# Kernel optimization log

Measured on AMD Instinct MI355X. Metric: run time of the kernel, lower is better.

## Reference

```python
import jax, jax.numpy as jnp
import numpy as np

B, T, D_IN, D_OUT = 128, 2048, 128, 256


def setup_inputs() -> dict:
    key = jax.random.key(0)
    ks = jax.random.split(key, 8)
    s_in = 1.0 / np.sqrt(D_IN)
    s_h = 1.0 / np.sqrt(D_OUT)
    def orth(k):
        a = jax.random.normal(k, (D_OUT, D_OUT), dtype=jnp.float32)
        q, _ = jnp.linalg.qr(a)
        return q.astype(jnp.float32)
    return {
        "x": jax.random.normal(ks[0], (B, T, D_IN), dtype=jnp.float32),
        "h0": jnp.zeros((B, D_OUT), dtype=jnp.float32),
        "Wz": jax.random.normal(ks[1], (D_IN, D_OUT), dtype=jnp.float32) * s_in,
        "Wr": jax.random.normal(ks[2], (D_IN, D_OUT), dtype=jnp.float32) * s_in,
        "Wx": jax.random.normal(ks[3], (D_IN, D_OUT), dtype=jnp.float32) * s_in,
        "Uh": orth(ks[4]),
        "Rz": orth(ks[5]),
        "Rr": orth(ks[6]),
        "Bz": jnp.zeros((D_OUT,), dtype=jnp.float32),
        "Br": jnp.zeros((D_OUT,), dtype=jnp.float32),
        "Bh": jnp.zeros((D_OUT,), dtype=jnp.float32),
    }


def _mod_relu(zi, bi):
    # zi / |zi| * relu(|zi| + bi)  (faithful to the original modReLU)
    a = jnp.abs(zi)
    return zi / a * jax.nn.relu(a + bi)


def reference(x, h0, Wz, Wr, Wx, Uh, Rz, Rr, Bz, Br, Bh):
    # Precompute input projections for all timesteps in three big GEMMs.
    xz = jnp.einsum('btd,dh->bth', x, Wz) + Bz  # [B,T,H]
    xr = jnp.einsum('btd,dh->bth', x, Wr) + Br
    xx = jnp.einsum('btd,dh->bth', x, Wx)

    def step(h, xs):
        xz_t, xr_t, xx_t = xs
        zt = jax.nn.sigmoid(xz_t + h @ Rz)
        rt = jax.nn.sigmoid(xr_t + h @ Rr)
        zi = xx_t + rt * (h @ Uh)
        h_new = zt * h + (1.0 - zt) * _mod_relu(zi, Bh)
        return h_new, h_new

    # scan over time: move T to leading axis
    xs = (jnp.swapaxes(xz, 0, 1), jnp.swapaxes(xr, 0, 1), jnp.swapaxes(xx, 0, 1))
    _, ys = jax.lax.scan(step, h0, xs)  # ys: [T,B,H]
    return jnp.swapaxes(ys, 0, 1)  # [B,T,H]
```

## Files before the change

### kernel.cpp

```cpp
#include <hip/hip_runtime.h>
#include <math.h>

#define B_   128
#define T_   2048
#define DIN  128
#define H_   256

__device__ __forceinline__ void f4fma(float4& a, float s, const float4& w) {
  a.x = fmaf(s, w.x, a.x);
  a.y = fmaf(s, w.y, a.y);
  a.z = fmaf(s, w.z, a.z);
  a.w = fmaf(s, w.w, a.w);
}

__global__ __launch_bounds__(256, 3) void proj_kernel(
    const float* __restrict__ x,
    const float* __restrict__ Wz, const float* __restrict__ Wr, const float* __restrict__ Wx,
    const float* __restrict__ Bz, const float* __restrict__ Br,
    float* __restrict__ xout, int t0, int Tc)
{
  __shared__ float xs[32 * DIN];
  __shared__ float ws[32 * H_];
  const int tid = threadIdx.x;
  const int c0  = tid & 63;
  const int rg  = tid >> 6;
  const int rt  = blockIdx.x;
  const int ct  = blockIdx.y;
  const float* Wm = (ct == 0) ? Wz : (ct == 1) ? Wr : Wx;

  const int R0   = rt * 32;
  const int bb   = R0 / Tc;
  const int tau0 = R0 - bb * Tc;
  const float* xsrc = x + ((size_t)bb * T_ + t0 + tau0) * DIN;

  #pragma unroll
  for (int u = 0; u < 4; ++u) {
    int id = tid + 256 * u;
    *(float4*)&xs[4 * id] = *(const float4*)&xsrc[4 * id];
  }

  float4 acc[8];
  #pragma unroll
  for (int r = 0; r < 8; ++r) acc[r] = make_float4(0.f, 0.f, 0.f, 0.f);

  for (int ks = 0; ks < DIN; ks += 32) {
    __syncthreads();
    #pragma unroll
    for (int u = 0; u < 8; ++u) {
      int id = tid + 256 * u;
      int row = id >> 6, col4 = id & 63;
      *(float4*)&ws[4 * id] = *(const float4*)&Wm[(size_t)(ks + row) * H_ + 4 * col4];
    }
    __syncthreads();
    #pragma unroll
    for (int kk = 0; kk < 32; kk += 4) {
      float4 xv[8];
      #pragma unroll
      for (int r = 0; r < 8; ++r)
        xv[r] = *(const float4*)&xs[(8 * rg + r) * DIN + ks + kk];
      #pragma unroll
      for (int u = 0; u < 4; ++u) {
        float4 wv = *(const float4*)&ws[(kk + u) * H_ + 4 * c0];
        #pragma unroll
        for (int r = 0; r < 8; ++r) {
          float s = (u == 0) ? xv[r].x : (u == 1) ? xv[r].y : (u == 2) ? xv[r].z : xv[r].w;
          f4fma(acc[r], s, wv);
        }
      }
    }
  }

  float4 bias = make_float4(0.f, 0.f, 0.f, 0.f);
  if (ct == 0)      bias = *(const float4*)&Bz[4 * c0];
  else if (ct == 1) bias = *(const float4*)&Br[4 * c0];

  #pragma unroll
  for (int r = 0; r < 8; ++r) {
    int R = R0 + 8 * rg + r;
    float4 v = acc[r];
    v.x += bias.x; v.y += bias.y; v.z += bias.z; v.w += bias.w;
    *(float4*)&xout[(size_t)R * 768 + ct * H_ + 4 * c0] = v;
  }
}

__global__ __launch_bounds__(512, 2) void scan_kernel(
    const float* __restrict__ xproj,
    const float* __restrict__ Rz, const float* __restrict__ Rr,
    const float* __restrict__ Uh, const float* __restrict__ Bh,
    const float* __restrict__ h0,
    float* __restrict__ hcarry, float* __restrict__ out,
    int t0, int Tc)
{
  extern __shared__ float smem[];
  float* uh_lds = smem;
  float* pA = uh_lds + 15 * 8 * H_;
  float* pB = pA + 2048;
  float* pC = pB + 2048;
  float* hb = pC + 2048;
  float* xb = hb + H_;

  const int tid = threadIdx.x;
  const int g   = tid & 63;
  const int kb  = tid >> 6;
  const int k0  = kb * 32;
  const int g4  = 4 * g;
  const int b   = blockIdx.x;

  const float* xp = xproj + (size_t)b * Tc * 768;
  float* outp = out + ((size_t)b * T_ + t0) * H_;

  float4 wz[28], wu[17];
  #pragma unroll
  for (int i = 0; i < 28; ++i) wz[i] = *(const float4*)&Rz[(size_t)(k0 + i) * H_ + g4];
  #pragma unroll
  for (int i = 0; i < 17; ++i) wu[i] = *(const float4*)&Uh[(size_t)(k0 + i) * H_ + g4];
  #pragma unroll
  for (int i = 0; i < 15; ++i) {
    float4 v = *(const float4*)&Uh[(size_t)(k0 + 17 + i) * H_ + g4];
    *(float4*)&uh_lds[(kb * 15 + i) * H_ + g4] = v;
  }

  float bh_j = 0.f;
  if (tid < H_) {
    hb[tid] = (t0 == 0) ? h0[b * H_ + tid] : hcarry[b * H_ + tid];
    bh_j = Bh[tid];
  }
  float4 xcur = make_float4(0.f, 0.f, 0.f, 0.f);
  if (tid < 192) xcur = *(const float4*)&xp[4 * tid];
  __syncthreads();
  if (tid < 192) *(float4*)&xb[4 * tid] = xcur;

  int parity = 0;

  for (int tau = 0; tau < Tc; ++tau) {
    int blind = 0;
    asm volatile("" : "+v"(blind));
    const float* RzB = Rz + blind;
    const float* RrB = Rr + blind;

    float4 xnext = make_float4(0.f, 0.f, 0.f, 0.f);
    const bool dox = (tid < 192) && (tau + 1 < Tc);
    if (dox) xnext = *(const float4*)&xp[(size_t)(tau + 1) * 768 + 4 * tid];

    float4 bufA[4], bufB[4];
    #pragma unroll
    for (int i = 0; i < 4; ++i) bufA[i] = *(const float4*)&RzB[(size_t)(k0 + 28 + i) * H_ + g4];
    #pragma unroll
    for (int i = 0; i < 4; ++i) bufB[i] = *(const float4*)&RrB[(size_t)(k0 + i) * H_ + g4];

    float4 accZ = make_float4(0.f,0.f,0.f,0.f);
    float4 accR = make_float4(0.f,0.f,0.f,0.f);
    float4 accU = make_float4(0.f,0.f,0.f,0.f);

    #pragma unroll
    for (int i = 0; i < 7; ++i) f4fma(accZ, hb[k0 + i], wz[i]);
    #pragma unroll
    for (int i = 0; i < 4; ++i) f4fma(accZ, hb[k0 + 28 + i], bufA[i]);
    #pragma unroll
    for (int i = 0; i < 4; ++i) bufA[i] = *(const float4*)&RrB[(size_t)(k0 + 4 + i) * H_ + g4];
    #pragma unroll
    for (int i = 7; i < 14; ++i) f4fma(accZ, hb[k0 + i], wz[i]);
    #pragma unroll
    for (int i = 0; i < 4; ++i) f4fma(accR, hb[k0 + i], bufB[i]);
    #pragma unroll
    for (int i = 0; i < 4; ++i) bufB[i] = *(const float4*)&RrB[(size_t)(k0 + 8 + i) * H_ + g4];
    #pragma unroll
    for (int i = 14; i < 21; ++i) f4fma(accZ, hb[k0 + i], wz[i]);
    #pragma unroll
    for (int i = 0; i < 4; ++i) f4fma(accR, hb[k0 + 4 + i], bufA[i]);
    #pragma unroll
    for (int i = 0; i < 4; ++i) bufA[i] = *(const float4*)&RrB[(size_t)(k0 + 12 + i) * H_ + g4];
    #pragma unroll
    for (int i = 21; i < 28; ++i) f4fma(accZ, hb[k0 + i], wz[i]);
    #pragma unroll
    for (int i = 0; i < 4; ++i) f4fma(accR, hb[k0 + 8 + i], bufB[i]);
    #pragma unroll
    for (int i = 0; i < 4; ++i) bufB[i] = *(const float4*)&RrB[(size_t)(k0 + 16 + i) * H_ + g4];
    #pragma unroll
    for (int i = 0; i < 9; ++i) f4fma(accU, hb[k0 + i], wu[i]);
    #pragma unroll
    for (int i = 0; i < 4; ++i) f4fma(accR, hb[k0 + 12 + i], bufA[i]);
    #pragma unroll
    for (int i = 0; i < 4; ++i) bufA[i] = *(const float4*)&RrB[(size_t)(k0 + 20 + i) * H_ + g4];
    #pragma unroll
    for (int i = 9; i < 17; ++i) f4fma(accU, hb[k0 + i], wu[i]);
    #pragma unroll
    for (int i = 0; i < 4; ++i) f4fma(accR, hb[k0 + 16 + i], bufB[i]);
    #pragma unroll
    for (int i = 0; i < 4; ++i) bufB[i] = *(const float4*)&RrB[(size_t)(k0 + 24 + i) * H_ + g4];
    #pragma unroll
    for (int i = 0; i < 8; ++i) {
      float4 w = *(const float4*)&uh_lds[(kb * 15 + i) * H_ + g4];
      f4fma(accU, hb[k0 + 17 + i], w);
    }
    #pragma unroll
    for (int i = 0; i < 4; ++i) f4fma(accR, hb[k0 + 20 + i], bufA[i]);
    #pragma unroll
    for (int i = 0; i < 4; ++i) bufA[i] = *(const float4*)&RrB[(size_t)(k0 + 28 + i) * H_ + g4];
    #pragma unroll
    for (int i = 8; i < 15; ++i) {
      float4 w = *(const float4*)&uh_lds[(kb * 15 + i) * H_ + g4];
      f4fma(accU, hb[k0 + 17 + i], w);
    }
    #pragma unroll
    for (int i = 0; i < 4; ++i) f4fma(accR, hb[k0 + 24 + i], bufB[i]);
    #pragma unroll
    for (int i = 0; i < 4; ++i) f4fma(accR, hb[k0 + 28 + i], bufA[i]);

    *(float4*)&pA[4 * tid] = accZ;
    *(float4*)&pB[4 * tid] = accR;
    *(float4*)&pC[4 * tid] = accU;
    if (dox) *(float4*)&xb[(parity ^ 1) * 768 + 4 * tid] = xnext;
    __syncthreads();

    if (tid < H_) {
      const int j = tid;
      float sz = xb[parity * 768 + j];
      float sr = xb[parity * 768 + H_ + j];
      float su = 0.f;
      #pragma unroll
      for (int q = 0; q < 8; ++q) {
        sz += pA[q * 256 + j];
        sr += pB[q * 256 + j];
        su += pC[q * 256 + j];
      }
      float zt = 1.f / (1.f + expf(-sz));
      float rt = 1.f / (1.f + expf(-sr));
      float zi = xb[parity * 768 + 2 * H_ + j] + rt * su;
      float a = fabsf(zi);
      float relu_v = fmaxf(a + bh_j, 0.f);
      float mr = (zi / a) * relu_v;
      float hold = hb[j];
      float hn = zt * hold + (1.f - zt) * mr;
      outp[(size_t)tau * H_ + j] = hn;
      hb[j] = hn;
    }
    __syncthreads();
    parity ^= 1;
  }

  if (tid < H_) hcarry[b * H_ + tid] = hb[tid];
}

extern "C" void kernel_launch(void* const* d_in, const int* in_sizes, int n_in,
                              void* d_out, int out_size, void* d_ws, size_t ws_size,
                              hipStream_t stream)
{
  const float* x  = (const float*)d_in[0];
  const float* h0 = (const float*)d_in[1];
  const float* Wz = (const float*)d_in[2];
  const float* Wr = (const float*)d_in[3];
  const float* Wx = (const float*)d_in[4];
  const float* Uh = (const float*)d_in[5];
  const float* Rz = (const float*)d_in[6];
  const float* Rr = (const float*)d_in[7];
  const float* Bz = (const float*)d_in[8];
  const float* Br = (const float*)d_in[9];
  const float* Bh = (const float*)d_in[10];
  float* out = (float*)d_out;

  float* hcarry = (float*)d_ws;
  float* xproj  = (float*)d_ws + 32768;

  int Tc = 32;
  const int cands[7] = {2048, 1024, 512, 256, 128, 64, 32};
  for (int i = 0; i < 7; ++i) {
    size_t need = 131072 + (size_t)cands[i] * 128 * 768 * 4;
    if (need <= ws_size) { Tc = cands[i]; break; }
  }

  const int SMEM = (15 * 8 * 256 + 3 * 2048 + 256 + 2 * 768) * 4;
  (void)hipFuncSetAttribute((const void*)scan_kernel,
                            hipFuncAttributeMaxDynamicSharedMemorySize, SMEM);

  const int nch = T_ / Tc;
  for (int c = 0; c < nch; ++c) {
    int t0 = c * Tc;
    dim3 g1(128 * Tc / 32, 3);
    proj_kernel<<<g1, 256, 0, stream>>>(x, Wz, Wr, Wx, Bz, Br, xproj, t0, Tc);
    scan_kernel<<<128, 512, SMEM, stream>>>(xproj, Rz, Rr, Uh, Bh, h0,
                                            hcarry, out, t0, Tc);
  }
}
```

Baseline: 9.879 ms.

## Split each batch row's scan across two blocks with flag-based h exchange

```diff
diff --git a/kernel.cpp b/kernel.cpp
--- a/kernel.cpp
+++ b/kernel.cpp
@@ -5,6 +5,15 @@
 #define T_   2048
 #define DIN  128
 #define H_   256
+
+typedef float fx4 __attribute__((ext_vector_type(4)));
+
+__device__ __forceinline__ void vfma(fx4& a, float s, fx4 w) {
+  a.x = fmaf(s, w.x, a.x);
+  a.y = fmaf(s, w.y, a.y);
+  a.z = fmaf(s, w.z, a.z);
+  a.w = fmaf(s, w.w, a.w);
+}
 
 __device__ __forceinline__ void f4fma(float4& a, float s, const float4& w) {
   a.x = fmaf(s, w.x, a.x);
@@ -89,157 +98,125 @@
     const float* __restrict__ Uh, const float* __restrict__ Bh,
     const float* __restrict__ h0,
     float* __restrict__ hcarry, float* __restrict__ out,
+    float* __restrict__ comm, int* __restrict__ flags,
     int t0, int Tc)
 {
-  extern __shared__ float smem[];
-  float* uh_lds = smem;
-  float* pA = uh_lds + 15 * 8 * H_;
-  float* pB = pA + 2048;
-  float* pC = pB + 2048;
-  float* hb = pC + 2048;
-  float* xb = hb + H_;
-
-  const int tid = threadIdx.x;
-  const int g   = tid & 63;
-  const int kb  = tid >> 6;
-  const int k0  = kb * 32;
-  const int g4  = 4 * g;
-  const int b   = blockIdx.x;
+  __shared__ fx4 pZ[512], pR[512], pU[512];
+  __shared__ float hbuf[2][H_];
+
+  const int tid  = threadIdx.x;
+  const int b    = blockIdx.x >> 1;
+  const int half = blockIdx.x & 1;
+  const int g    = tid & 31;
+  const int kb   = tid >> 5;
+  const int cbase = half * 128 + 4 * g;
+  const bool kLocal = ((kb >> 3) == half);
+  const bool fetcher = (kb == (half ? 0 : 8));
+  const int myid  = b * 2 + half;
+  const int othid = b * 2 + (1 - half);
 
   const float* xp = xproj + (size_t)b * Tc * 768;
   float* outp = out + ((size_t)b * T_ + t0) * H_;
 
-  float4 wz[28], wu[17];
-  #pragma unroll
-  for (int i = 0; i < 28; ++i) wz[i] = *(const float4*)&Rz[(size_t)(k0 + i) * H_ + g4];
-  #pragma unroll
-  for (int i = 0; i < 17; ++i) wu[i] = *(const float4*)&Uh[(size_t)(k0 + i) * H_ + g4];
-  #pragma unroll
-  for (int i = 0; i < 15; ++i) {
-    float4 v = *(const float4*)&Uh[(size_t)(k0 + 17 + i) * H_ + g4];
-    *(float4*)&uh_lds[(kb * 15 + i) * H_ + g4] = v;
+  fx4 rz[16], rr[16], ru[16];
+  #pragma unroll
+  for (int i = 0; i < 16; ++i) {
+    const size_t row = (size_t)(kb * 16 + i) * H_ + cbase;
+    rz[i] = *(const fx4*)&Rz[row];
+    rr[i] = *(const fx4*)&Rr[row];
+    ru[i] = *(const fx4*)&Uh[row];
+  }
+  #pragma unroll
+  for (int i = 0; i < 16; ++i) {
+    asm volatile("" : "+v"(rz[i]));
+    asm volatile("" : "+v"(rr[i]));
+    asm volatile("" : "+v"(ru[i]));
   }
 
   float bh_j = 0.f;
-  if (tid < H_) {
-    hb[tid] = (t0 == 0) ? h0[b * H_ + tid] : hcarry[b * H_ + tid];
-    bh_j = Bh[tid];
-  }
-  float4 xcur = make_float4(0.f, 0.f, 0.f, 0.f);
-  if (tid < 192) xcur = *(const float4*)&xp[4 * tid];
+  if (tid < 128) bh_j = Bh[half * 128 + tid];
+
+  const float* hsrc = (t0 == 0) ? (h0 + (size_t)b * H_) : (hcarry + (size_t)b * H_);
+  if (tid < 64) *(fx4*)&hbuf[0][4 * tid] = *(const fx4*)&hsrc[4 * tid];
   __syncthreads();
-  if (tid < 192) *(float4*)&xb[4 * tid] = xcur;
-
-  int parity = 0;
-
+
+  int p = 0;
+  #pragma unroll 1
   for (int tau = 0; tau < Tc; ++tau) {
-    int blind = 0;
-    asm volatile("" : "+v"(blind));
-    const float* RzB = Rz + blind;
-    const float* RrB = Rr + blind;
-
-    float4 xnext = make_float4(0.f, 0.f, 0.f, 0.f);
-    const bool dox = (tid < 192) && (tau + 1 < Tc);
-    if (dox) xnext = *(const float4*)&xp[(size_t)(tau + 1) * 768 + 4 * tid];
-
-    float4 bufA[4], bufB[4];
-    #pragma unroll
-    for (int i = 0; i < 4; ++i) bufA[i] = *(const float4*)&RzB[(size_t)(k0 + 28 + i) * H_ + g4];
-    #pragma unroll
-    for (int i = 0; i < 4; ++i) bufB[i] = *(const float4*)&RrB[(size_t)(k0 + i) * H_ + g4];
-
-    float4 accZ = make_float4(0.f,0.f,0.f,0.f);
-    float4 accR = make_float4(0.f,0.f,0.f,0.f);
-    float4 accU = make_float4(0.f,0.f,0.f,0.f);
-
-    #pragma unroll
-    for (int i = 0; i < 7; ++i) f4fma(accZ, hb[k0 + i], wz[i]);
-    #pragma unroll
-    for (int i = 0; i < 4; ++i) f4fma(accZ, hb[k0 + 28 + i], bufA[i]);
-    #pragma unroll
-    for (int i = 0; i < 4; ++i) bufA[i] = *(const float4*)&RrB[(size_t)(k0 + 4 + i) * H_ + g4];
-    #pragma unroll
-    for (int i = 7; i < 14; ++i) f4fma(accZ, hb[k0 + i], wz[i]);
-    #pragma unroll
-    for (int i = 0; i < 4; ++i) f4fma(accR, hb[k0 + i], bufB[i]);
-    #pragma unroll
-    for (int i = 0; i < 4; ++i) bufB[i] = *(const float4*)&RrB[(size_t)(k0 + 8 + i) * H_ + g4];
-    #pragma unroll
-    for (int i = 14; i < 21; ++i) f4fma(accZ, hb[k0 + i], wz[i]);
-    #pragma unroll
-    for (int i = 0; i < 4; ++i) f4fma(accR, hb[k0 + 4 + i], bufA[i]);
-    #pragma unroll
-    for (int i = 0; i < 4; ++i) bufA[i] = *(const float4*)&RrB[(size_t)(k0 + 12 + i) * H_ + g4];
-    #pragma unroll
-    for (int i = 21; i < 28; ++i) f4fma(accZ, hb[k0 + i], wz[i]);
-    #pragma unroll
-    for (int i = 0; i < 4; ++i) f4fma(accR, hb[k0 + 8 + i], bufB[i]);
-    #pragma unroll
-    for (int i = 0; i < 4; ++i) bufB[i] = *(const float4*)&RrB[(size_t)(k0 + 16 + i) * H_ + g4];
-    #pragma unroll
-    for (int i = 0; i < 9; ++i) f4fma(accU, hb[k0 + i], wu[i]);
-    #pragma unroll
-    for (int i = 0; i < 4; ++i) f4fma(accR, hb[k0 + 12 + i], bufA[i]);
-    #pragma unroll
-    for (int i = 0; i < 4; ++i) bufA[i] = *(const float4*)&RrB[(size_t)(k0 + 20 + i) * H_ + g4];
-    #pragma unroll
-    for (int i = 9; i < 17; ++i) f4fma(accU, hb[k0 + i], wu[i]);
-    #pragma unroll
-    for (int i = 0; i < 4; ++i) f4fma(accR, hb[k0 + 16 + i], bufB[i]);
-    #pragma unroll
-    for (int i = 0; i < 4; ++i) bufB[i] = *(const float4*)&RrB[(size_t)(k0 + 24 + i) * H_ + g4];
-    #pragma unroll
-    for (int i = 0; i < 8; ++i) {
-      float4 w = *(const float4*)&uh_lds[(kb * 15 + i) * H_ + g4];
-      f4fma(accU, hb[k0 + 17 + i], w);
-    }
-    #pragma unroll
-    for (int i = 0; i < 4; ++i) f4fma(accR, hb[k0 + 20 + i], bufA[i]);
-    #pragma unroll
-    for (int i = 0; i < 4; ++i) bufA[i] = *(const float4*)&RrB[(size_t)(k0 + 28 + i) * H_ + g4];
-    #pragma unroll
-    for (int i = 8; i < 15; ++i) {
-      float4 w = *(const float4*)&uh_lds[(kb * 15 + i) * H_ + g4];
-      f4fma(accU, hb[k0 + 17 + i], w);
-    }
-    #pragma unroll
-    for (int i = 0; i < 4; ++i) f4fma(accR, hb[k0 + 24 + i], bufB[i]);
-    #pragma unroll
-    for (int i = 0; i < 4; ++i) f4fma(accR, hb[k0 + 28 + i], bufA[i]);
-
-    *(float4*)&pA[4 * tid] = accZ;
-    *(float4*)&pB[4 * tid] = accR;
-    *(float4*)&pC[4 * tid] = accU;
-    if (dox) *(float4*)&xb[(parity ^ 1) * 768 + 4 * tid] = xnext;
-    __syncthreads();
-
-    if (tid < H_) {
-      const int j = tid;
-      float sz = xb[parity * 768 + j];
-      float sr = xb[parity * 768 + H_ + j];
-      float su = 0.f;
-      #pragma unroll
-      for (int q = 0; q < 8; ++q) {
-        sz += pA[q * 256 + j];
-        sr += pB[q * 256 + j];
-        su += pC[q * 256 + j];
+    float xzv = 0.f, xrv = 0.f, xxv = 0.f;
+    if (tid < 128) {
+      const float* xt = xp + (size_t)tau * 768 + half * 128 + tid;
+      xzv = xt[0]; xrv = xt[256]; xxv = xt[512];
+    }
+
+    fx4 az = {0.f, 0.f, 0.f, 0.f};
+    fx4 ar = {0.f, 0.f, 0.f, 0.f};
+    fx4 au = {0.f, 0.f, 0.f, 0.f};
+
+    auto do_fmas = [&]() {
+      #pragma unroll
+      for (int u = 0; u < 4; ++u) {
+        fx4 h4 = *(const fx4*)&hbuf[p][kb * 16 + 4 * u];
+        vfma(az, h4.x, rz[4*u+0]); vfma(ar, h4.x, rr[4*u+0]); vfma(au, h4.x, ru[4*u+0]);
+        vfma(az, h4.y, rz[4*u+1]); vfma(ar, h4.y, rr[4*u+1]); vfma(au, h4.y, ru[4*u+1]);
+        vfma(az, h4.z, rz[4*u+2]); vfma(ar, h4.z, rr[4*u+2]); vfma(au, h4.z, ru[4*u+2]);
+        vfma(az, h4.w, rz[4*u+3]); vfma(ar, h4.w, rr[4*u+3]); vfma(au, h4.w, ru[4*u+3]);
+      }
+      pZ[tid] = az; pR[tid] = ar; pU[tid] = au;
+    };
+
+    if (kLocal) do_fmas();
+
+    if (fetcher && tau > 0) {
+      const int slot = p ^ 1;
+      const int want = t0 + tau;
+      const int fidx = othid * 2 + slot;
+      while (__hip_atomic_load(&flags[fidx], __ATOMIC_ACQUIRE, __HIP_MEMORY_SCOPE_AGENT) < want) { }
+      const float* src = comm + (size_t)(othid * 2 + slot) * 128 + 4 * g;
+      float v0 = __hip_atomic_load(&src[0], __ATOMIC_RELAXED, __HIP_MEMORY_SCOPE_AGENT);
+      float v1 = __hip_atomic_load(&src[1], __ATOMIC_RELAXED, __HIP_MEMORY_SCOPE_AGENT);
+      float v2 = __hip_atomic_load(&src[2], __ATOMIC_RELAXED, __HIP_MEMORY_SCOPE_AGENT);
+      float v3 = __hip_atomic_load(&src[3], __ATOMIC_RELAXED, __HIP_MEMORY_SCOPE_AGENT);
+      float* dst = &hbuf[p][(1 - half) * 128 + 4 * g];
+      dst[0] = v0; dst[1] = v1; dst[2] = v2; dst[3] = v3;
+    }
+    __syncthreads();
+
+    if (!kLocal) do_fmas();
+    __syncthreads();
+
+    if (tid < 128) {
+      const float* fZ = (const float*)pZ;
+      const float* fR = (const float*)pR;
+      const float* fU = (const float*)pU;
+      float sz = xzv, sr = xrv, su = 0.f;
+      #pragma unroll
+      for (int q = 0; q < 16; ++q) {
+        sz += fZ[q * 128 + tid];
+        sr += fR[q * 128 + tid];
+        su += fU[q * 128 + tid];
       }
       float zt = 1.f / (1.f + expf(-sz));
       float rt = 1.f / (1.f + expf(-sr));
-      float zi = xb[parity * 768 + 2 * H_ + j] + rt * su;
-      float a = fabsf(zi);
-      float relu_v = fmaxf(a + bh_j, 0.f);
-      float mr = (zi / a) * relu_v;
-      float hold = hb[j];
+      float zi = xxv + rt * su;
+      float a  = fabsf(zi);
+      float mr = (zi / a) * fmaxf(a + bh_j, 0.f);
+      float hold = hbuf[p][half * 128 + tid];
       float hn = zt * hold + (1.f - zt) * mr;
-      outp[(size_t)tau * H_ + j] = hn;
-      hb[j] = hn;
-    }
-    __syncthreads();
-    parity ^= 1;
-  }
-
-  if (tid < H_) hcarry[b * H_ + tid] = hb[tid];
+      outp[(size_t)tau * H_ + half * 128 + tid] = hn;
+      hbuf[p ^ 1][half * 128 + tid] = hn;
+      __hip_atomic_store(&comm[(size_t)(myid * 2 + p) * 128 + tid], hn,
+                         __ATOMIC_RELAXED, __HIP_MEMORY_SCOPE_AGENT);
+    }
+    __syncthreads();
+
+    if (tid == 0)
+      __hip_atomic_store(&flags[myid * 2 + p], t0 + tau + 1,
+                         __ATOMIC_RELEASE, __HIP_MEMORY_SCOPE_AGENT);
+    p ^= 1;
+  }
+
+  if (tid < 128) hcarry[(size_t)b * H_ + half * 128 + tid] = hbuf[0][half * 128 + tid];
 }
 
 extern "C" void kernel_launch(void* const* d_in, const int* in_sizes, int n_in,
@@ -260,25 +237,25 @@
   float* out = (float*)d_out;
 
   float* hcarry = (float*)d_ws;
-  float* xproj  = (float*)d_ws + 32768;
+  float* comm   = (float*)((char*)d_ws + 131072);
+  int*   flags  = (int*)((char*)d_ws + 131072 + 262144);
+  float* xproj  = (float*)((char*)d_ws + 1048576);
+
+  hipMemsetAsync(flags, 0, 512 * sizeof(int), stream);
 
   int Tc = 32;
   const int cands[7] = {2048, 1024, 512, 256, 128, 64, 32};
   for (int i = 0; i < 7; ++i) {
-    size_t need = 131072 + (size_t)cands[i] * 128 * 768 * 4;
+    size_t need = 1048576 + (size_t)cands[i] * 128 * 768 * 4;
     if (need <= ws_size) { Tc = cands[i]; break; }
   }
-
-  const int SMEM = (15 * 8 * 256 + 3 * 2048 + 256 + 2 * 768) * 4;
-  (void)hipFuncSetAttribute((const void*)scan_kernel,
-                            hipFuncAttributeMaxDynamicSharedMemorySize, SMEM);
 
   const int nch = T_ / Tc;
   for (int c = 0; c < nch; ++c) {
     int t0 = c * Tc;
     dim3 g1(128 * Tc / 32, 3);
     proj_kernel<<<g1, 256, 0, stream>>>(x, Wz, Wr, Wx, Bz, Br, xproj, t0, Tc);
-    scan_kernel<<<128, 512, SMEM, stream>>>(xproj, Rz, Rr, Uh, Bh, h0,
-                                            hcarry, out, t0, Tc);
-  }
-}
+    scan_kernel<<<256, 512, 0, stream>>>(xproj, Rz, Rr, Uh, Bh, h0,
+                                         hcarry, out, comm, flags, t0, Tc);
+  }
+}
```

Result: slower. 18.71 ms (+89.4%).
